# Performance work log

Measured on AMD Instinct MI355X. Metric: run time of the kernel, lower is better.

## Reference

```python
import jax, jax.numpy as jnp
import numpy as np

H, D = 8, 16            # heads, per-head dim (hidden_channels // heads)
HID = H * D             # 128
N_MAT, N_ELEM = 100000, 118
F_MAT, F_ELEM = 128, 64
OUT = 64
E_EM, E_MM = 1000000, 2000000
NEG_SLOPE = 0.2

def _k(i):
    return jax.random.fold_in(jax.random.key(0), i)

def setup_inputs() -> dict:
    p = lambda i, shape: 0.1 * jax.random.normal(_k(i), shape, dtype=jnp.float32)
    return dict(
        x_mat=jax.random.normal(_k(0), (N_MAT, F_MAT), dtype=jnp.float32),
        x_elem=jax.random.normal(_k(1), (N_ELEM, F_ELEM), dtype=jnp.float32),
        W_proj_mat=p(2, (HID, F_MAT)), b_proj_mat=p(3, (HID,)),
        W_proj_elem=p(4, (HID, F_ELEM)), b_proj_elem=p(5, (HID,)),
        a_src_em=p(6, (H, D)), a_dst_em=p(7, (H, D)),
        a_src_mm=p(8, (H, D)), a_dst_mm=p(9, (H, D)),
        Wk=p(10, (HID, HID)), bk=p(11, (HID,)), q=p(12, (HID,)),
        Wl=p(13, (OUT, HID)), bl=p(14, (OUT,)),
        src_em=jax.random.randint(_k(15), (E_EM,), 0, N_ELEM, dtype=jnp.int32),
        dst_em=jax.random.randint(_k(16), (E_EM,), 0, N_MAT, dtype=jnp.int32),
        src_mm=jax.random.randint(_k(17), (E_MM,), 0, N_MAT, dtype=jnp.int32),
        dst_mm=jax.random.randint(_k(18), (E_MM,), 0, N_MAT, dtype=jnp.int32),
    )

def _edge_type_conv(x_s, x_d, a_s, a_d, src, dst, n_dst):
    # x_s:[Ns,H,D], x_d:[Nd,H,D]; per-edge-type GAT-style attention (HANConv.message)
    alpha = jnp.sum(x_s * a_s, -1)[src] + jnp.sum(x_d * a_d, -1)[dst]   # [E,H]
    alpha = jax.nn.leaky_relu(alpha, NEG_SLOPE)
    amax = jax.ops.segment_max(alpha, dst, num_segments=n_dst)          # stable softmax per dst
    ex = jnp.exp(alpha - amax[dst])
    den = jax.ops.segment_sum(ex, dst, num_segments=n_dst)
    w = ex / (den[dst] + 1e-16)                                         # [E,H]
    out = jax.ops.segment_sum(x_s[src] * w[:, :, None], dst, num_segments=n_dst)  # [Nd,H,D]
    return jax.nn.relu(out.reshape(n_dst, HID))

def _group(xs, q, Wk, bk):
    # HANConv semantic-level attention over metapaths
    s = jnp.stack(xs)                                                   # [M,N,C]
    score = jnp.sum(q * jnp.mean(jnp.tanh(s @ Wk.T + bk), axis=1), axis=-1)  # [M]
    attn = jax.nn.softmax(score)
    return jnp.einsum('m,mnc->nc', attn, s)

def reference(x_mat, x_elem, W_proj_mat, b_proj_mat, W_proj_elem, b_proj_elem,
              a_src_em, a_dst_em, a_src_mm, a_dst_mm, Wk, bk, q, Wl, bl,
              src_em, dst_em, src_mm, dst_mm):
    h_mat = (x_mat @ W_proj_mat.T + b_proj_mat).reshape(N_MAT, H, D)
    h_elem = (x_elem @ W_proj_elem.T + b_proj_elem).reshape(N_ELEM, H, D)
    o_em = _edge_type_conv(h_elem, h_mat, a_src_em, a_dst_em, src_em, dst_em, N_MAT)
    o_mm = _edge_type_conv(h_mat, h_mat, a_src_mm, a_dst_mm, src_mm, dst_mm, N_MAT)
    out_mat = _group([o_em, o_mm], q, Wk, bk)                           # [N_MAT, HID]
    return out_mat @ Wl.T + bl                                          # final Linear
```

## Files before the change

### kernel.cpp

```cpp
#include <hip/hip_runtime.h>
#include <hip/hip_bf16.h>

typedef unsigned int uint32;
typedef unsigned short ushort16;

using bf16x8 = __attribute__((ext_vector_type(8))) short;
using f32x4  = __attribute__((ext_vector_type(4))) float;

#define N_MATN 100000
#define N_ELEMN 118
#define F_MATN 128
#define F_ELEMN 64
#define HIDN 128
#define NHEAD 8
#define OUTC 64
#define SCORE_BLOCKS 1024
#define NSTRIPS 6250
#define NT2 16
#define NTILES2 (N_MATN/NT2)

#define SH 8
#define NBK 391
#define BCH 8192

__device__ __forceinline__ float blo(uint32 u){ return __uint_as_float(u << 16); }
__device__ __forceinline__ float bhi(uint32 u){ return __uint_as_float(u & 0xffff0000u); }
__device__ __forceinline__ ushort16 f2bf(float f){
    uint32 u = __float_as_uint(f);
    uint32 r = u + 0x7FFFu + ((u >> 16) & 1u);
    return (ushort16)(r >> 16);
}
__device__ __forceinline__ uint32 pack2(float a, float b){
    return (uint32)f2bf(a) | ((uint32)f2bf(b) << 16);
}
__device__ __forceinline__ bf16x8 cvt8(const float* __restrict__ p){
    bf16x8 r;
    #pragma unroll
    for(int j=0;j<8;j++) r[j] = (short)f2bf(p[j]);
    return r;
}

__global__ __launch_bounds__(128) void proj_elem_v2(
    const float* __restrict__ x, const float* __restrict__ W,
    const float* __restrict__ bias, const float* __restrict__ a_se,
    ushort16* __restrict__ h, float* __restrict__ asrc_em)
{
    __shared__ float xr[F_ELEMN];
    int n = blockIdx.x, c = threadIdx.x;
    if(c < 16) ((float4*)xr)[c] = ((const float4*)(x + n*F_ELEMN))[c];
    __syncthreads();
    const float4* Wr = (const float4*)(W + c*F_ELEMN);
    float acc = 0.f;
    #pragma unroll 4
    for(int i=0;i<16;i++){
        float4 w = Wr[i];
        acc += xr[4*i]*w.x + xr[4*i+1]*w.y + xr[4*i+2]*w.z + xr[4*i+3]*w.w;
    }
    acc += bias[c];
    h[n*HIDN + c] = f2bf(acc);
    float p = acc * a_se[c];
    #pragma unroll
    for(int m=8;m>=1;m>>=1) p += __shfl_xor(p, m, 16);
    if((c&15)==0) asrc_em[n*NHEAD + (c>>4)] = p;
}

__global__ __launch_bounds__(256) void proj_mat_mfma(
    const float* __restrict__ x, const float* __restrict__ W,
    const float* __restrict__ bias,
    const float* __restrict__ a_de, const float* __restrict__ a_sm, const float* __restrict__ a_dm,
    ushort16* __restrict__ h,
    float* __restrict__ adst_em, float* __restrict__ asrc_mm, float* __restrict__ adst_mm)
{
    int tid = threadIdx.x;
    int wv = tid >> 6, lane = tid & 63, quad = lane >> 4, sl = lane & 15;
    bf16x8 B[2][4];
    float bc[2], ade[2], asv[2], adv[2];
    #pragma unroll
    for(int i=0;i<2;i++){
        int c = (2*wv+i)*16 + sl;
        const float* wr = W + c*F_MATN;
        #pragma unroll
        for(int ks=0;ks<4;ks++) B[i][ks] = cvt8(wr + ks*32 + quad*8);
        bc[i] = bias[c]; ade[i] = a_de[c]; asv[i] = a_sm[c]; adv[i] = a_dm[c];
    }
    for(int s = blockIdx.x; s < NSTRIPS; s += gridDim.x){
        int n0 = s*16;
        const float* xrow = x + (size_t)(n0+sl)*F_MATN;
        bf16x8 A[4];
        #pragma unroll
        for(int ks=0;ks<4;ks++) A[ks] = cvt8(xrow + ks*32 + quad*8);
        f32x4 acc[2];
        #pragma unroll
        for(int i=0;i<2;i++){ acc[i][0]=0.f; acc[i][1]=0.f; acc[i][2]=0.f; acc[i][3]=0.f; }
        #pragma unroll
        for(int i=0;i<2;i++)
            #pragma unroll
            for(int ks=0;ks<4;ks++)
                acc[i] = __builtin_amdgcn_mfma_f32_16x16x32_bf16(A[ks], B[i][ks], acc[i], 0, 0, 0);
        #pragma unroll
        for(int i=0;i<2;i++){
            int head = 2*wv + i;
            #pragma unroll
            for(int r=0;r<4;r++){
                float a = acc[i][r] + bc[i];
                int node = n0 + quad*4 + r;
                h[(size_t)node*HIDN + head*16 + sl] = f2bf(a);
                float p0 = a*ade[i], p1 = a*asv[i], p2 = a*adv[i];
                #pragma unroll
                for(int m=8;m>=1;m>>=1){
                    p0 += __shfl_xor(p0, m);
                    p1 += __shfl_xor(p1, m);
                    p2 += __shfl_xor(p2, m);
                }
                if(sl == 0){
                    adst_em[node*NHEAD + head] = p0;
                    asrc_mm[node*NHEAD + head] = p1;
                    adst_mm[node*NHEAD + head] = p2;
                }
            }
        }
    }
}

__global__ __launch_bounds__(256) void bucket_count(
    const int* __restrict__ dst_em, int nE_em, int* __restrict__ bcnt_em,
    const int* __restrict__ dst_mm, int nE_mm, int* __restrict__ bcnt_mm)
{
    __shared__ int he[NBK], hm[NBK];
    int t = threadIdx.x;
    for(int i=t;i<NBK;i+=256){ he[i]=0; hm[i]=0; }
    __syncthreads();
    int gt = blockIdx.x*256 + t;
    int st = gridDim.x*256;
    {
        int n4 = nE_em >> 2;
        const int4* d4 = (const int4*)dst_em;
        for(int i = gt; i < n4; i += st){
            int4 v = d4[i];
            atomicAdd(&he[v.x>>SH],1); atomicAdd(&he[v.y>>SH],1);
            atomicAdd(&he[v.z>>SH],1); atomicAdd(&he[v.w>>SH],1);
        }
        for(int i = (n4<<2) + gt; i < nE_em; i += st) atomicAdd(&he[dst_em[i]>>SH],1);
    }
    {
        int n4 = nE_mm >> 2;
        const int4* d4 = (const int4*)dst_mm;
        for(int i = gt; i < n4; i += st){
            int4 v = d4[i];
            atomicAdd(&hm[v.x>>SH],1); atomicAdd(&hm[v.y>>SH],1);
            atomicAdd(&hm[v.z>>SH],1); atomicAdd(&hm[v.w>>SH],1);
        }
        for(int i = (n4<<2) + gt; i < nE_mm; i += st) atomicAdd(&hm[dst_mm[i]>>SH],1);
    }
    __syncthreads();
    for(int j=t;j<NBK;j+=256){
        int a = he[j], b = hm[j];
        if(a) atomicAdd(&bcnt_em[j], a);
        if(b) atomicAdd(&bcnt_mm[j], b);
    }
}

__global__ __launch_bounds__(512) void bucket_scan(
    const int* __restrict__ bcnt_em, int* __restrict__ bb_em, int* __restrict__ bcur_em,
    const int* __restrict__ bcnt_mm, int* __restrict__ bb_mm, int* __restrict__ bcur_mm,
    int* __restrict__ offs_em, int* __restrict__ offs_mm, int nE_em, int nE_mm)
{
    __shared__ int wsum[8];
    int t = threadIdx.x, l = t & 63, w = t >> 6;
    {
        int v = (t < NBK) ? bcnt_em[t] : 0;
        int x = v;
        #pragma unroll
        for(int off=1; off<64; off<<=1){ int y = __shfl_up(x, off); if(l >= off) x += y; }
        if(l == 63) wsum[w] = x;
        __syncthreads();
        int base = 0;
        for(int k=0;k<w;k++) base += wsum[k];
        int excl = base + x - v;
        if(t < NBK){ bb_em[t] = excl; bcur_em[t] = excl; }
        if(t == 0){ bb_em[NBK] = nE_em; offs_em[N_MATN] = nE_em; }
        __syncthreads();
    }
    {
        int v = (t < NBK) ? bcnt_mm[t] : 0;
        int x = v;
        #pragma unroll
        for(int off=1; off<64; off<<=1){ int y = __shfl_up(x, off); if(l >= off) x += y; }
        if(l == 63) wsum[w] = x;
        __syncthreads();
        int base = 0;
        for(int k=0;k<w;k++) base += wsum[k];
        int excl = base + x - v;
        if(t < NBK){ bb_mm[t] = excl; bcur_mm[t] = excl; }
        if(t == 0){ bb_mm[NBK] = nE_mm; offs_mm[N_MATN] = nE_mm; }
    }
}

__global__ __launch_bounds__(256) void bin_pass(
    const int* __restrict__ src_em, const int* __restrict__ dst_em, int nE_em,
    int* __restrict__ bcur_em, uint32* __restrict__ st_em,
    const int* __restrict__ src_mm, const int* __restrict__ dst_mm, int nE_mm,
    int* __restrict__ bcur_mm, uint32* __restrict__ st_mm)
{
    __shared__ int cnt[NBK];
    __shared__ int base[NBK];
    int t = threadIdx.x;
    int nch_em = (nE_em + BCH - 1)/BCH;
    int nch_mm = (nE_mm + BCH - 1)/BCH;
    int ntot = nch_em + nch_mm;
    for(int c = blockIdx.x; c < ntot; c += gridDim.x){
        bool em = c < nch_em;
        const int* src = em ? src_em : src_mm;
        const int* dst = em ? dst_em : dst_mm;
        int nE   = em ? nE_em : nE_mm;
        int* bcur = em ? bcur_em : bcur_mm;
        uint32* st = em ? st_em : st_mm;
        int cc = em ? c : c - nch_em;
        int s = cc*BCH;
        int e = s + BCH; if(e > nE) e = nE;
        int len = e - s;
        int n4 = len >> 2;
        const int4* d4 = (const int4*)(dst + s);
        const int4* s4 = (const int4*)(src + s);
        for(int i=t;i<NBK;i+=256) cnt[i] = 0;
        __syncthreads();
        for(int i=t;i<n4;i+=256){
            int4 v = d4[i];
            atomicAdd(&cnt[v.x>>SH],1); atomicAdd(&cnt[v.y>>SH],1);
            atomicAdd(&cnt[v.z>>SH],1); atomicAdd(&cnt[v.w>>SH],1);
        }
        for(int i = s + (n4<<2) + t; i < e; i += 256) atomicAdd(&cnt[dst[i]>>SH], 1);
        __syncthreads();
        for(int i=t;i<NBK;i+=256){
            int v = cnt[i];
            base[i] = v ? atomicAdd(&bcur[i], v) : 0;
            cnt[i] = 0;
        }
        __syncthreads();
        for(int i=t;i<n4;i+=256){
            int4 dv = d4[i];
            int4 sv = s4[i];
            int b, p;
            b = dv.x>>SH; p = base[b] + atomicAdd(&cnt[b],1);
            st[p] = ((uint32)(dv.x & ((1<<SH)-1)) << 17) | (uint32)sv.x;
            b = dv.y>>SH; p = base[b] + atomicAdd(&cnt[b],1);
            st[p] = ((uint32)(dv.y & ((1<<SH)-1)) << 17) | (uint32)sv.y;
            b = dv.z>>SH; p = base[b] + atomicAdd(&cnt[b],1);
            st[p] = ((uint32)(dv.z & ((1<<SH)-1)) << 17) | (uint32)sv.z;
            b = dv.w>>SH; p = base[b] + atomicAdd(&cnt[b],1);
            st[p] = ((uint32)(dv.w & ((1<<SH)-1)) << 17) | (uint32)sv.w;
        }
        for(int i = s + (n4<<2) + t; i < e; i += 256){
            int d = dst[i];
            int b = d >> SH;
            int p = base[b] + atomicAdd(&cnt[b], 1);
            st[p] = ((uint32)(d & ((1<<SH)-1)) << 17) | (uint32)src[i];
        }
        __syncthreads();
    }
}

__global__ __launch_bounds__(256) void place_pass(
    const int* __restrict__ bb_em, const uint32* __restrict__ st_em,
    int* __restrict__ csr_em, int* __restrict__ offs_em,
    const int* __restrict__ bb_mm, const uint32* __restrict__ st_mm,
    int* __restrict__ csr_mm, int* __restrict__ offs_mm)
{
    __shared__ int cnt[256];
    __shared__ int wsum[4];
    __shared__ int cur[256];
    int b = blockIdx.x;
    bool em = b < NBK;
    const int* bb        = em ? bb_em : bb_mm;
    const uint32* stp    = em ? st_em : st_mm;
    int* csr             = em ? csr_em : csr_mm;
    int* offs            = em ? offs_em : offs_mm;
    int bk = em ? b : b - NBK;
    int d0 = bk << SH;
    int t = threadIdx.x, l = t & 63, w = t >> 6;
    int nd = N_MATN - d0; if(nd > 256) nd = 256;
    int beg = bb[bk], end = bb[bk+1];
    cnt[t] = 0;
    __syncthreads();
    for(int i = beg + t; i < end; i += 256)
        atomicAdd(&cnt[stp[i] >> 17], 1);
    __syncthreads();
    int v = cnt[t];
    int x = v;
    #pragma unroll
    for(int off=1; off<64; off<<=1){ int y = __shfl_up(x, off); if(l >= off) x += y; }
    if(l == 63) wsum[w] = x;
    __syncthreads();
    int base = beg;
    for(int k=0;k<w;k++) base += wsum[k];
    int excl = base + x - v;
    cur[t] = excl;
    if(t < nd) offs[d0 + t] = excl;
    __syncthreads();
    for(int i = beg + t; i < end; i += 256){
        uint32 vv = stp[i];
        int dl = (int)(vv >> 17);
        int p = atomicAdd(&cur[dl], 1);
        csr[p] = (int)(vv & 0x1FFFFu);
    }
}

__global__ __launch_bounds__(256) void agg_both(
    const int* __restrict__ offs_em, const int* __restrict__ csr_em,
    const ushort16* __restrict__ h_elem, const float* __restrict__ asrc_em,
    const float* __restrict__ adst_em, ushort16* __restrict__ o_em,
    const int* __restrict__ offs_mm, const int* __restrict__ csr_mm,
    const ushort16* __restrict__ h_mat, const float* __restrict__ asrc_mm,
    const float* __restrict__ adst_mm, ushort16* __restrict__ o_mm)
{
    int lane = threadIdx.x & 63;
    int g = lane >> 4;
    int q = lane & 15;
    int hd = q >> 1;
    int w = (blockIdx.x*blockDim.x + threadIdx.x) >> 6;
    int nw = (gridDim.x*blockDim.x) >> 6;
    for(int nid = w; nid < 2*N_MATN; nid += nw){
        int nidu = __builtin_amdgcn_readfirstlane(nid);
        bool em = nidu < N_MATN;
        int d = em ? nidu : nidu - N_MATN;
        const int*    offs = em ? offs_em : offs_mm;
        const int*    csr  = em ? csr_em  : csr_mm;
        const uint32* hs   = (const uint32*)(em ? h_elem : h_mat);
        const float*  asp  = em ? asrc_em : asrc_mm;
        const float*  adp  = em ? adst_em : adst_mm;
        uint32*       op   = (uint32*)(em ? o_em : o_mm);
        int beg = offs[d], end = offs[d+1];
        float ad = adp[(unsigned)(d*NHEAD + hd)];
        float denA = 0.f, denB = 0.f;
        float nloA[4] = {0.f,0.f,0.f,0.f}, nhiA[4] = {0.f,0.f,0.f,0.f};
        float nloB[4] = {0.f,0.f,0.f,0.f}, nhiB[4] = {0.f,0.f,0.f,0.f};
        for(int j0 = beg; j0 < end; j0 += 8){
            int e0 = j0 + g, e1 = j0 + 4 + g;
            bool v0 = e0 < end, v1 = e1 < end;
            int s0 = csr[(unsigned)(v0 ? e0 : end - 1)];
            int s1 = csr[(unsigned)(v1 ? e1 : end - 1)];
            float a0 = asp[(unsigned)(s0*NHEAD + hd)];
            float a1 = asp[(unsigned)(s1*NHEAD + hd)];
            const uint4 h0 = *(const uint4*)(hs + (unsigned)(s0*64 + q*4));
            const uint4 h1 = *(const uint4*)(hs + (unsigned)(s1*64 + q*4));
            float al0 = a0 + ad; al0 = fmaxf(al0, 0.2f*al0);
            float ex0 = __expf(al0); ex0 = v0 ? ex0 : 0.f;
            float al1 = a1 + ad; al1 = fmaxf(al1, 0.2f*al1);
            float ex1 = __expf(al1); ex1 = v1 ? ex1 : 0.f;
            denA += ex0; denB += ex1;
            nloA[0] += blo(h0.x)*ex0; nhiA[0] += bhi(h0.x)*ex0;
            nloA[1] += blo(h0.y)*ex0; nhiA[1] += bhi(h0.y)*ex0;
            nloA[2] += blo(h0.z)*ex0; nhiA[2] += bhi(h0.z)*ex0;
            nloA[3] += blo(h0.w)*ex0; nhiA[3] += bhi(h0.w)*ex0;
            nloB[0] += blo(h1.x)*ex1; nhiB[0] += bhi(h1.x)*ex1;
            nloB[1] += blo(h1.y)*ex1; nhiB[1] += bhi(h1.y)*ex1;
            nloB[2] += blo(h1.z)*ex1; nhiB[2] += bhi(h1.z)*ex1;
            nloB[3] += blo(h1.w)*ex1; nhiB[3] += bhi(h1.w)*ex1;
        }
        float den = denA + denB;
        den += __shfl_xor(den, 16); den += __shfl_xor(den, 32);
        float nlo[4], nhi[4];
        #pragma unroll
        for(int k=0;k<4;k++){
            nlo[k] = nloA[k] + nloB[k];
            nhi[k] = nhiA[k] + nhiB[k];
            nlo[k] += __shfl_xor(nlo[k], 16); nlo[k] += __shfl_xor(nlo[k], 32);
            nhi[k] += __shfl_xor(nhi[k], 16); nhi[k] += __shfl_xor(nhi[k], 32);
        }
        if(g == 0){
            float rdn = 1.0f/(den + 1e-16f);
            uint4 pk;
            pk.x = pack2(fmaxf(nlo[0]*rdn, 0.f), fmaxf(nhi[0]*rdn, 0.f));
            pk.y = pack2(fmaxf(nlo[1]*rdn, 0.f), fmaxf(nhi[1]*rdn, 0.f));
            pk.z = pack2(fmaxf(nlo[2]*rdn, 0.f), fmaxf(nhi[2]*rdn, 0.f));
            pk.w = pack2(fmaxf(nlo[3]*rdn, 0.f), fmaxf(nhi[3]*rdn, 0.f));
            *(uint4*)(op + (size_t)d*64 + q*4) = pk;
        }
    }
}

__global__ __launch_bounds__(256) void score_mfma(
    const ushort16* __restrict__ o_em, const ushort16* __restrict__ o_mm,
    const float* __restrict__ Wk, const float* __restrict__ bkv,
    const float* __restrict__ qv, float* __restrict__ partials)
{
    int tid = threadIdx.x;
    int wv = tid >> 6, lane = tid & 63, quad = lane >> 4, sl = lane & 15;
    bf16x8 B[2][4];
    float bkc[2], qc[2];
    #pragma unroll
    for(int i=0;i<2;i++){
        int c = (2*wv+i)*16 + sl;
        const float* wr = Wk + c*HIDN;
        #pragma unroll
        for(int ks=0;ks<4;ks++) B[i][ks] = cvt8(wr + ks*32 + quad*8);
        bkc[i] = bkv[c]; qc[i] = qv[c];
    }
    float se = 0.f, sm = 0.f;
    for(int s = blockIdx.x; s < NSTRIPS; s += gridDim.x){
        int n0 = s*16;
        const bf16x8* rowE = (const bf16x8*)(o_em + (size_t)(n0+sl)*HIDN);
        const bf16x8* rowM = (const bf16x8*)(o_mm + (size_t)(n0+sl)*HIDN);
        bf16x8 AE[4], AM[4];
        #pragma unroll
        for(int ks=0;ks<4;ks++){
            AE[ks] = rowE[ks*4 + quad];
            AM[ks] = rowM[ks*4 + quad];
        }
        f32x4 aE[2], aM[2];
        #pragma unroll
        for(int i=0;i<2;i++){
            aE[i][0]=0.f;aE[i][1]=0.f;aE[i][2]=0.f;aE[i][3]=0.f;
            aM[i][0]=0.f;aM[i][1]=0.f;aM[i][2]=0.f;aM[i][3]=0.f;
        }
        #pragma unroll
        for(int i=0;i<2;i++)
            #pragma unroll
            for(int ks=0;ks<4;ks++){
                aE[i] = __builtin_amdgcn_mfma_f32_16x16x32_bf16(AE[ks], B[i][ks], aE[i], 0, 0, 0);
                aM[i] = __builtin_amdgcn_mfma_f32_16x16x32_bf16(AM[ks], B[i][ks], aM[i], 0, 0, 0);
            }
        #pragma unroll
        for(int i=0;i<2;i++)
            #pragma unroll
            for(int r=0;r<4;r++){
                se += qc[i]*tanhf(aE[i][r] + bkc[i]);
                sm += qc[i]*tanhf(aM[i][r] + bkc[i]);
            }
    }
    #pragma unroll
    for(int m=32;m>=1;m>>=1){ se += __shfl_xor(se,m); sm += __shfl_xor(sm,m); }
    __shared__ float red[8];
    if(lane==0){ red[wv*2]=se; red[wv*2+1]=sm; }
    __syncthreads();
    if(tid==0){
        partials[blockIdx.x*2+0] = red[0]+red[2]+red[4]+red[6];
        partials[blockIdx.x*2+1] = red[1]+red[3]+red[5]+red[7];
    }
}

__global__ __launch_bounds__(256) void reduce_scores_kernel(
    const float* __restrict__ partials, float* __restrict__ scores)
{
    __shared__ float sh0[256], sh1[256];
    int t = threadIdx.x;
    float s0=0.f, s1=0.f;
    for(int i=t;i<SCORE_BLOCKS;i+=256){ s0 += partials[2*i]; s1 += partials[2*i+1]; }
    sh0[t]=s0; sh1[t]=s1; __syncthreads();
    for(int s=128;s>0;s>>=1){ if(t<s){ sh0[t]+=sh0[t+s]; sh1[t]+=sh1[t+s]; } __syncthreads(); }
    if(t==0){ scores[0]=sh0[0]; scores[1]=sh1[0]; }
}

__global__ __launch_bounds__(256) void final_v4(
    const ushort16* __restrict__ o_em, const ushort16* __restrict__ o_mm,
    const float* __restrict__ Wl, const float* __restrict__ blv,
    const float* __restrict__ scores, float* __restrict__ out)
{
    __shared__ float wlds[64*129];
    __shared__ float zlds[NT2*128];
    int t = threadIdx.x;
    for(int i=t;i<2048;i+=256){
        float4 v = ((const float4*)Wl)[i];
        int r = i >> 5, k4 = i & 31;
        float* d = wlds + r*129 + k4*4;
        d[0]=v.x; d[1]=v.y; d[2]=v.z; d[3]=v.w;
    }
    float s0 = scores[0]*(1.0f/N_MATN), s1 = scores[1]*(1.0f/N_MATN);
    float mx = fmaxf(s0,s1);
    float e0 = __expf(s0-mx), e1 = __expf(s1-mx);
    float inv = 1.0f/(e0+e1);
    float a0 = e0*inv, a1 = e1*inv;
    int j = t & 63, half = t >> 6;
    float bj = blv[j];
    const float* wr = wlds + j*129;
    __syncthreads();
    for(int tile = blockIdx.x; tile < NTILES2; tile += gridDim.x){
        int n0 = tile*NT2;
        __syncthreads();
        {
            const uint4* pe = (const uint4*)((const uint32*)o_em + (size_t)n0*64);
            const uint4* pm = (const uint4*)((const uint32*)o_mm + (size_t)n0*64);
            uint4 ve = pe[t], vm = pm[t];
            float* zd = zlds + t*8;
            zd[0]=a0*blo(ve.x)+a1*blo(vm.x); zd[1]=a0*bhi(ve.x)+a1*bhi(vm.x);
            zd[2]=a0*blo(ve.y)+a1*blo(vm.y); zd[3]=a0*bhi(ve.y)+a1*bhi(vm.y);
            zd[4]=a0*blo(ve.z)+a1*blo(vm.z); zd[5]=a0*bhi(ve.z)+a1*bhi(vm.z);
            zd[6]=a0*blo(ve.w)+a1*blo(vm.w); zd[7]=a0*bhi(ve.w)+a1*bhi(vm.w);
        }
        __syncthreads();
        float acc[4] = {0.f,0.f,0.f,0.f};
        #pragma unroll 1
        for(int kk=0;kk<128;kk+=8){
            float f0=wr[kk],f1=wr[kk+1],f2=wr[kk+2],f3=wr[kk+3];
            float f4=wr[kk+4],f5=wr[kk+5],f6=wr[kk+6],f7=wr[kk+7];
            #pragma unroll
            for(int n=0;n<4;n++){
                const float4* zr = (const float4*)(zlds + (half*4+n)*128 + kk);
                float4 za = zr[0], zb = zr[1];
                acc[n] += za.x*f0 + za.y*f1 + za.z*f2 + za.w*f3
                        + zb.x*f4 + zb.y*f5 + zb.z*f6 + zb.w*f7;
            }
        }
        #pragma unroll
        for(int n=0;n<4;n++)
            out[(size_t)(n0 + half*4 + n)*OUTC + j] = bj + acc[n];
    }
}

extern "C" void kernel_launch(void* const* d_in, const int* in_sizes, int n_in,
                              void* d_out, int out_size, void* d_ws, size_t ws_size,
                              hipStream_t stream)
{
    const float* x_mat    = (const float*)d_in[0];
    const float* x_elem   = (const float*)d_in[1];
    const float* W_pm     = (const float*)d_in[2];
    const float* b_pm     = (const float*)d_in[3];
    const float* W_pe     = (const float*)d_in[4];
    const float* b_pe     = (const float*)d_in[5];
    const float* a_se     = (const float*)d_in[6];
    const float* a_de     = (const float*)d_in[7];
    const float* a_sm     = (const float*)d_in[8];
    const float* a_dm     = (const float*)d_in[9];
    const float* Wk       = (const float*)d_in[10];
    const float* bk       = (const float*)d_in[11];
    const float* qv       = (const float*)d_in[12];
    const float* Wl       = (const float*)d_in[13];
    const float* bl       = (const float*)d_in[14];
    const int* src_em     = (const int*)d_in[15];
    const int* dst_em     = (const int*)d_in[16];
    const int* src_mm     = (const int*)d_in[17];
    const int* dst_mm     = (const int*)d_in[18];
    int nE_em = in_sizes[15];
    int nE_mm = in_sizes[17];

    char* ws = (char*)d_ws;
    size_t off = 0;
    auto alloc = [&](size_t bytes) -> void* {
        void* p = ws + off; off += (bytes + 255) & ~size_t(255); return p;
    };
    ushort16* h_mat   = (ushort16*)alloc((size_t)N_MATN*HIDN*2);
    ushort16* h_elem  = (ushort16*)alloc((size_t)N_ELEMN*HIDN*2);
    float*    asrcEM  = (float*)   alloc((size_t)N_ELEMN*NHEAD*4);
    float*    adstEM  = (float*)   alloc((size_t)N_MATN*NHEAD*4);
    float*    asrcMM  = (float*)   alloc((size_t)N_MATN*NHEAD*4);
    float*    adstMM  = (float*)   alloc((size_t)N_MATN*NHEAD*4);
    int*      offs_em = (int*)     alloc((size_t)(N_MATN+1)*4);
    int*      offs_mm = (int*)     alloc((size_t)(N_MATN+1)*4);
    int*      csr_em  = (int*)     alloc((size_t)1000000*4);
    int*      csr_mm  = (int*)     alloc((size_t)2000000*4);
    ushort16* o_em    = (ushort16*)alloc((size_t)N_MATN*HIDN*2);
    ushort16* o_mm    = (ushort16*)alloc((size_t)N_MATN*HIDN*2);
    float*    partials= (float*)   alloc((size_t)SCORE_BLOCKS*2*4);
    float*    scores  = (float*)   alloc(256);
    int*      bb_em   = (int*)     alloc((size_t)(NBK+1)*4);
    int*      bb_mm   = (int*)     alloc((size_t)(NBK+1)*4);
    int*      bcur_em = (int*)     alloc((size_t)NBK*4);
    int*      bcur_mm = (int*)     alloc((size_t)NBK*4);
    size_t zero_start = off;
    int*      bcnt_em = (int*)     alloc((size_t)NBK*4);
    int*      bcnt_mm = (int*)     alloc((size_t)NBK*4);
    size_t zero_bytes = off - zero_start;

    uint32* st_em = (uint32*)o_em;
    uint32* st_mm = st_em + nE_em;

    hipMemsetAsync(ws + zero_start, 0, zero_bytes, stream);

    proj_elem_v2<<<N_ELEMN, 128, 0, stream>>>(x_elem, W_pe, b_pe, a_se, h_elem, asrcEM);
    proj_mat_mfma<<<1024, 256, 0, stream>>>(x_mat, W_pm, b_pm, a_de, a_sm, a_dm,
                                            h_mat, adstEM, asrcMM, adstMM);

    bucket_count<<<256, 256, 0, stream>>>(dst_em, nE_em, bcnt_em, dst_mm, nE_mm, bcnt_mm);
    bucket_scan<<<1, 512, 0, stream>>>(bcnt_em, bb_em, bcur_em,
                                       bcnt_mm, bb_mm, bcur_mm,
                                       offs_em, offs_mm, nE_em, nE_mm);

    int nch = (nE_em + BCH - 1)/BCH + (nE_mm + BCH - 1)/BCH;
    bin_pass<<<nch, 256, 0, stream>>>(src_em, dst_em, nE_em, bcur_em, st_em,
                                      src_mm, dst_mm, nE_mm, bcur_mm, st_mm);
    place_pass<<<2*NBK, 256, 0, stream>>>(bb_em, st_em, csr_em, offs_em,
                                          bb_mm, st_mm, csr_mm, offs_mm);

    agg_both<<<4096, 256, 0, stream>>>(offs_em, csr_em, h_elem, asrcEM, adstEM, o_em,
                                       offs_mm, csr_mm, h_mat, asrcMM, adstMM, o_mm);

    score_mfma<<<SCORE_BLOCKS, 256, 0, stream>>>(o_em, o_mm, Wk, bk, qv, partials);
    reduce_scores_kernel<<<1, 256, 0, stream>>>(partials, scores);
    final_v4<<<2048, 256, 0, stream>>>(o_em, o_mm, Wl, bl, scores, (float*)d_out);
}
```

Measured before the change: 460.2 us.

## Merge projection kernels, atomic score reduction, packed FMA aggregation, larger bin chunks

After: 476.4 us. 1.04x slower.

```diff
diff --git a/kernel.cpp b/kernel.cpp
--- a/kernel.cpp
+++ b/kernel.cpp
@@ -6,6 +6,7 @@
 
 using bf16x8 = __attribute__((ext_vector_type(8))) short;
 using f32x4  = __attribute__((ext_vector_type(4))) float;
+using f32x2  = __attribute__((ext_vector_type(2))) float;
 
 #define N_MATN 100000
 #define N_ELEMN 118
@@ -14,14 +15,13 @@
 #define HIDN 128
 #define NHEAD 8
 #define OUTC 64
-#define SCORE_BLOCKS 1024
 #define NSTRIPS 6250
 #define NT2 16
 #define NTILES2 (N_MATN/NT2)
 
 #define SH 8
 #define NBK 391
-#define BCH 8192
+#define BCH 16384
 
 __device__ __forceinline__ float blo(uint32 u){ return __uint_as_float(u << 16); }
 __device__ __forceinline__ float bhi(uint32 u){ return __uint_as_float(u & 0xffff0000u); }
@@ -40,38 +40,45 @@
     return r;
 }
 
-__global__ __launch_bounds__(128) void proj_elem_v2(
-    const float* __restrict__ x, const float* __restrict__ W,
-    const float* __restrict__ bias, const float* __restrict__ a_se,
-    ushort16* __restrict__ h, float* __restrict__ asrc_em)
-{
-    __shared__ float xr[F_ELEMN];
-    int n = blockIdx.x, c = threadIdx.x;
-    if(c < 16) ((float4*)xr)[c] = ((const float4*)(x + n*F_ELEMN))[c];
-    __syncthreads();
-    const float4* Wr = (const float4*)(W + c*F_ELEMN);
-    float acc = 0.f;
-    #pragma unroll 4
-    for(int i=0;i<16;i++){
-        float4 w = Wr[i];
-        acc += xr[4*i]*w.x + xr[4*i+1]*w.y + xr[4*i+2]*w.z + xr[4*i+3]*w.w;
-    }
-    acc += bias[c];
-    h[n*HIDN + c] = f2bf(acc);
-    float p = acc * a_se[c];
-    #pragma unroll
-    for(int m=8;m>=1;m>>=1) p += __shfl_xor(p, m, 16);
-    if((c&15)==0) asrc_em[n*NHEAD + (c>>4)] = p;
-}
-
-__global__ __launch_bounds__(256) void proj_mat_mfma(
+#define PKFMA(acc, u, e2) do{                                   \
+    f32x2 _hv; _hv[0] = blo(u); _hv[1] = bhi(u);                \
+    asm("v_pk_fma_f32 %0, %1, %2, %0"                           \
+        : "+v"(acc) : "v"(_hv), "v"(e2));                       \
+}while(0)
+
+__global__ __launch_bounds__(256) void proj_all(
+    const float* __restrict__ xe, const float* __restrict__ We,
+    const float* __restrict__ be, const float* __restrict__ a_se,
+    ushort16* __restrict__ h_elem, float* __restrict__ asrc_em,
     const float* __restrict__ x, const float* __restrict__ W,
     const float* __restrict__ bias,
     const float* __restrict__ a_de, const float* __restrict__ a_sm, const float* __restrict__ a_dm,
     ushort16* __restrict__ h,
     float* __restrict__ adst_em, float* __restrict__ asrc_mm, float* __restrict__ adst_mm)
 {
+    __shared__ float xr[F_ELEMN];
     int tid = threadIdx.x;
+    if(blockIdx.x < N_ELEMN){
+        int n = blockIdx.x, c = tid;
+        if(c < 16) ((float4*)xr)[c] = ((const float4*)(xe + n*F_ELEMN))[c];
+        __syncthreads();
+        if(c < 128){
+            const float4* Wr = (const float4*)(We + c*F_ELEMN);
+            float acc = 0.f;
+            #pragma unroll 4
+            for(int i=0;i<16;i++){
+                float4 w = Wr[i];
+                acc += xr[4*i]*w.x + xr[4*i+1]*w.y + xr[4*i+2]*w.z + xr[4*i+3]*w.w;
+            }
+            acc += be[c];
+            h_elem[n*HIDN + c] = f2bf(acc);
+            float p = acc * a_se[c];
+            #pragma unroll
+            for(int m=8;m>=1;m>>=1) p += __shfl_xor(p, m, 16);
+            if((c&15)==0) asrc_em[n*NHEAD + (c>>4)] = p;
+        }
+        return;
+    }
     int wv = tid >> 6, lane = tid & 63, quad = lane >> 4, sl = lane & 15;
     bf16x8 B[2][4];
     float bc[2], ade[2], asv[2], adv[2];
@@ -83,7 +90,8 @@
         for(int ks=0;ks<4;ks++) B[i][ks] = cvt8(wr + ks*32 + quad*8);
         bc[i] = bias[c]; ade[i] = a_de[c]; asv[i] = a_sm[c]; adv[i] = a_dm[c];
     }
-    for(int s = blockIdx.x; s < NSTRIPS; s += gridDim.x){
+    int nb = gridDim.x - N_ELEMN;
+    for(int s = blockIdx.x - N_ELEMN; s < NSTRIPS; s += nb){
         int n0 = s*16;
         const float* xrow = x + (size_t)(n0+sl)*F_MATN;
         bf16x8 A[4];
@@ -332,8 +340,9 @@
         int beg = offs[d], end = offs[d+1];
         float ad = adp[(unsigned)(d*NHEAD + hd)];
         float denA = 0.f, denB = 0.f;
-        float nloA[4] = {0.f,0.f,0.f,0.f}, nhiA[4] = {0.f,0.f,0.f,0.f};
-        float nloB[4] = {0.f,0.f,0.f,0.f}, nhiB[4] = {0.f,0.f,0.f,0.f};
+        f32x2 accA[4], accB[4];
+        #pragma unroll
+        for(int k=0;k<4;k++){ accA[k][0]=0.f; accA[k][1]=0.f; accB[k][0]=0.f; accB[k][1]=0.f; }
         for(int j0 = beg; j0 < end; j0 += 8){
             int e0 = j0 + g, e1 = j0 + 4 + g;
             bool v0 = e0 < end, v1 = e1 < end;
@@ -348,22 +357,20 @@
             float al1 = a1 + ad; al1 = fmaxf(al1, 0.2f*al1);
             float ex1 = __expf(al1); ex1 = v1 ? ex1 : 0.f;
             denA += ex0; denB += ex1;
-            nloA[0] += blo(h0.x)*ex0; nhiA[0] += bhi(h0.x)*ex0;
-            nloA[1] += blo(h0.y)*ex0; nhiA[1] += bhi(h0.y)*ex0;
-            nloA[2] += blo(h0.z)*ex0; nhiA[2] += bhi(h0.z)*ex0;
-            nloA[3] += blo(h0.w)*ex0; nhiA[3] += bhi(h0.w)*ex0;
-            nloB[0] += blo(h1.x)*ex1; nhiB[0] += bhi(h1.x)*ex1;
-            nloB[1] += blo(h1.y)*ex1; nhiB[1] += bhi(h1.y)*ex1;
-            nloB[2] += blo(h1.z)*ex1; nhiB[2] += bhi(h1.z)*ex1;
-            nloB[3] += blo(h1.w)*ex1; nhiB[3] += bhi(h1.w)*ex1;
+            f32x2 e20; e20[0]=ex0; e20[1]=ex0;
+            f32x2 e21; e21[0]=ex1; e21[1]=ex1;
+            PKFMA(accA[0], h0.x, e20); PKFMA(accA[1], h0.y, e20);
+            PKFMA(accA[2], h0.z, e20); PKFMA(accA[3], h0.w, e20);
+            PKFMA(accB[0], h1.x, e21); PKFMA(accB[1], h1.y, e21);
+            PKFMA(accB[2], h1.z, e21); PKFMA(accB[3], h1.w, e21);
         }
         float den = denA + denB;
         den += __shfl_xor(den, 16); den += __shfl_xor(den, 32);
         float nlo[4], nhi[4];
         #pragma unroll
         for(int k=0;k<4;k++){
-            nlo[k] = nloA[k] + nloB[k];
-            nhi[k] = nhiA[k] + nhiB[k];
+            nlo[k] = accA[k][0] + accB[k][0];
+            nhi[k] = accA[k][1] + accB[k][1];
             nlo[k] += __shfl_xor(nlo[k], 16); nlo[k] += __shfl_xor(nlo[k], 32);
             nhi[k] += __shfl_xor(nhi[k], 16); nhi[k] += __shfl_xor(nhi[k], 32);
         }
@@ -382,7 +389,7 @@
 __global__ __launch_bounds__(256) void score_mfma(
     const ushort16* __restrict__ o_em, const ushort16* __restrict__ o_mm,
     const float* __restrict__ Wk, const float* __restrict__ bkv,
-    const float* __restrict__ qv, float* __restrict__ partials)
+    const float* __restrict__ qv, float* __restrict__ scores)
 {
     int tid = threadIdx.x;
     int wv = tid >> 6, lane = tid & 63, quad = lane >> 4, sl = lane & 15;
@@ -434,21 +441,9 @@
     if(lane==0){ red[wv*2]=se; red[wv*2+1]=sm; }
     __syncthreads();
     if(tid==0){
-        partials[blockIdx.x*2+0] = red[0]+red[2]+red[4]+red[6];
-        partials[blockIdx.x*2+1] = red[1]+red[3]+red[5]+red[7];
-    }
-}
-
-__global__ __launch_bounds__(256) void reduce_scores_kernel(
-    const float* __restrict__ partials, float* __restrict__ scores)
-{
-    __shared__ float sh0[256], sh1[256];
-    int t = threadIdx.x;
-    float s0=0.f, s1=0.f;
-    for(int i=t;i<SCORE_BLOCKS;i+=256){ s0 += partials[2*i]; s1 += partials[2*i+1]; }
-    sh0[t]=s0; sh1[t]=s1; __syncthreads();
-    for(int s=128;s>0;s>>=1){ if(t<s){ sh0[t]+=sh0[t+s]; sh1[t]+=sh1[t+s]; } __syncthreads(); }
-    if(t==0){ scores[0]=sh0[0]; scores[1]=sh1[0]; }
+        atomicAdd(&scores[0], red[0]+red[2]+red[4]+red[6]);
+        atomicAdd(&scores[1], red[1]+red[3]+red[5]+red[7]);
+    }
 }
 
 __global__ __launch_bounds__(256) void final_v4(
@@ -550,8 +545,6 @@
     int*      csr_mm  = (int*)     alloc((size_t)2000000*4);
     ushort16* o_em    = (ushort16*)alloc((size_t)N_MATN*HIDN*2);
     ushort16* o_mm    = (ushort16*)alloc((size_t)N_MATN*HIDN*2);
-    float*    partials= (float*)   alloc((size_t)SCORE_BLOCKS*2*4);
-    float*    scores  = (float*)   alloc(256);
     int*      bb_em   = (int*)     alloc((size_t)(NBK+1)*4);
     int*      bb_mm   = (int*)     alloc((size_t)(NBK+1)*4);
     int*      bcur_em = (int*)     alloc((size_t)NBK*4);
@@ -559,6 +552,7 @@
     size_t zero_start = off;
     int*      bcnt_em = (int*)     alloc((size_t)NBK*4);
     int*      bcnt_mm = (int*)     alloc((size_t)NBK*4);
+    float*    scores  = (float*)   alloc(256);
     size_t zero_bytes = off - zero_start;
 
     uint32* st_em = (uint32*)o_em;
@@ -566,9 +560,10 @@
 
     hipMemsetAsync(ws + zero_start, 0, zero_bytes, stream);
 
-    proj_elem_v2<<<N_ELEMN, 128, 0, stream>>>(x_elem, W_pe, b_pe, a_se, h_elem, asrcEM);
-    proj_mat_mfma<<<1024, 256, 0, stream>>>(x_mat, W_pm, b_pm, a_de, a_sm, a_dm,
-                                            h_mat, adstEM, asrcMM, adstMM);
+    proj_all<<<1024 + N_ELEMN, 256, 0, stream>>>(
+        x_elem, W_pe, b_pe, a_se, h_elem, asrcEM,
+        x_mat, W_pm, b_pm, a_de, a_sm, a_dm,
+        h_mat, adstEM, asrcMM, adstMM);
 
     bucket_count<<<256, 256, 0, stream>>>(dst_em, nE_em, bcnt_em, dst_mm, nE_mm, bcnt_mm);
     bucket_scan<<<1, 512, 0, stream>>>(bcnt_em, bb_em, bcur_em,
@@ -584,7 +579,6 @@
     agg_both<<<4096, 256, 0, stream>>>(offs_em, csr_em, h_elem, asrcEM, adstEM, o_em,
                                        offs_mm, csr_mm, h_mat, asrcMM, adstMM, o_mm);
 
-    score_mfma<<<SCORE_BLOCKS, 256, 0, stream>>>(o_em, o_mm, Wk, bk, qv, partials);
-    reduce_scores_kernel<<<1, 256, 0, stream>>>(partials, scores);
+    score_mfma<<<1024, 256, 0, stream>>>(o_em, o_mm, Wk, bk, qv, scores);
     final_v4<<<2048, 256, 0, stream>>>(o_em, o_mm, Wl, bl, scores, (float*)d_out);
 }
```
